# Optimization experiments

Measured on AMD Instinct MI355X. Metric: run time of the kernel, lower is better.

## Reference

```python
import jax, jax.numpy as jnp
import numpy as np

N = 50000      # nodes
E = 800000     # edges (avg degree 16)
IN_DIM = 256
OUT_DIM = 256
H = 8          # heads
HD = OUT_DIM // H  # head_dim = 32


def setup_inputs() -> dict:
    key = jax.random.key(0)
    k = jax.random.split(key, 6)
    x = jax.random.normal(k[0], (N, IN_DIM), jnp.float32)
    edge_index = jax.random.randint(k[1], (2, E), 0, N, dtype=jnp.int64)
    s = 1.0 / np.sqrt(IN_DIM)
    W_src = jax.random.normal(k[2], (IN_DIM, OUT_DIM), jnp.float32) * s
    W_dst = jax.random.normal(k[3], (IN_DIM, OUT_DIM), jnp.float32) * s
    b_src = jnp.zeros((OUT_DIM,), jnp.float32)
    b_dst = jnp.zeros((OUT_DIM,), jnp.float32)
    # xavier-ish scale for [H, 2*HD] attention vector
    attn_vec = jax.random.normal(k[4], (H, 2 * HD), jnp.float32) * np.sqrt(2.0 / (H + 2 * HD))
    return {"x": x, "edge_index": edge_index, "W_src": W_src, "b_src": b_src,
            "W_dst": W_dst, "b_dst": b_dst, "attn_vec": attn_vec}


def reference(x, edge_index, W_src, b_src, W_dst, b_dst, attn_vec):
    # Linear projections -> [N, H, HD]
    proj_src = (x @ W_src + b_src).reshape(N, H, HD)
    proj_dst = (x @ W_dst + b_dst).reshape(N, H, HD)
    # Split concat-dot into two per-node dot products (same math as
    # einsum('ehd,hd->eh', cat([src,dst]), attn_vec)), computed per node
    # then gathered per edge.
    a_src, a_dst = attn_vec[:, :HD], attn_vec[:, HD:]
    s_src = jnp.einsum('nhd,hd->nh', proj_src, a_src)  # [N, H]
    s_dst = jnp.einsum('nhd,hd->nh', proj_dst, a_dst)  # [N, H]
    e_src, e_dst = edge_index[0], edge_index[1]
    scores = s_src[e_src] + s_dst[e_dst]               # [E, H]
    scores = jnp.where(scores >= 0, scores, 0.2 * scores)  # LeakyReLU(0.2)
    # Segment softmax over destination nodes (original: exp / scatter-add(exp) + eps)
    ex = jnp.exp(scores)
    denom = jax.ops.segment_sum(ex, e_dst, num_segments=N)  # [N, H]
    alpha = ex / (denom[e_dst] + 1e-15)                     # [E, H]
    # Weighted scatter aggregation of src features
    weighted = alpha[:, :, None] * proj_src[e_src]          # [E, H, HD]
    agg = jax.ops.segment_sum(weighted, e_dst, num_segments=N)  # [N, H, HD]
    # Single relation -> mean over messages is identity; residual add
    return x + agg.reshape(N, OUT_DIM)
```

## Files before the change

### kernel.cpp

```cpp
#include <hip/hip_runtime.h>

#define DIM 256
#define NHEAD 8
#define HDIM 32
#define NCHUNK 256
#define SLOT 64

typedef __attribute__((ext_vector_type(4))) float f32x4;
typedef __attribute__((ext_vector_type(8))) short short8;
typedef __attribute__((ext_vector_type(8))) __bf16 bf16x8;

static __device__ __forceinline__ unsigned short f2bf(float f) {
  unsigned int u = __float_as_uint(f);
  u = (u + 0x7fffu + ((u >> 16) & 1u)) >> 16;
  return (unsigned short)u;
}

static __device__ __forceinline__ f32x4 mfma16x16x32(short8 a, short8 b, f32x4 c) {
  union { short8 s; bf16x8 b; } ua, ub;
  ua.s = a; ub.s = b;
  return __builtin_amdgcn_mfma_f32_16x16x32_bf16(ua.b, ub.b, c, 0, 0, 0);
}

static __device__ __forceinline__ int edge_at(const void* ei, int is64, long long pos) {
  if (is64) return (int)((const long long*)ei)[pos];
  return ((const int*)ei)[pos];
}

static __device__ __forceinline__ int detect64(const void* ei, int E, int tid) {
  const unsigned int* raw = (const unsigned int*)ei;
  int chk = E < 256 ? E : 256;
  int bad = 0;
  for (int i = tid & 63; i < chk; i += 64) bad |= (raw[2 * i + 1] != 0u);
  return (__ballot(bad) == 0ull);
}

__global__ void __launch_bounds__(256) k_prep(const float* Wsrc, const float* Wdst,
                       const float* bsrc, const float* bdst, const float* attn,
                       float* c16, unsigned short* wp,
                       const void* ei, int E, int CS, unsigned int* cnt8, int nw) {
  __shared__ unsigned int hist[12800];
  int b = blockIdx.x, tid = threadIdx.x;
  if (b < 256) {
    int idx = b * 256 + tid;
    int k = idx >> 8, n = idx & 255;
    int kb = k >> 5, khi = (k >> 3) & 3, i = k & 7;
    int ct = n >> 4, lane = khi * 16 + (n & 15);
    wp[(((size_t)ct * 8 + kb) * 64 + lane) * 8 + i] = f2bf(Wsrc[(size_t)k * DIM + n]);
  } else if (b == 256) {
    for (int q = tid * 16, qe = q + 16; q < qe; ++q) {
      int kb = q >> 9, lane = (q >> 3) & 63, i = q & 7;
      int k = kb * 32 + ((lane >> 4) * 8) + i;
      int j = lane & 15;
      int h = j & 7;
      const float* W = (j < 8) ? Wsrc : Wdst;
      const float* a = attn + h * 2 * HDIM + ((j < 8) ? 0 : HDIM);
      float acc = 0.f;
      #pragma unroll
      for (int d = 0; d < HDIM; ++d)
        acc += W[(size_t)k * DIM + h * HDIM + d] * a[d];
      wp[(((size_t)16 * 8 + kb) * 64 + lane) * 8 + i] = f2bf(acc);
    }
    if (tid < 16) {
      int j = tid, h = j & 7;
      const float* bb = (j < 8) ? bsrc : bdst;
      const float* a = attn + h * 2 * HDIM + ((j < 8) ? 0 : HDIM);
      float c = 0.f;
      for (int d = 0; d < HDIM; ++d) c += bb[h * HDIM + d] * a[d];
      c16[j] = c;
    }
  } else {
    int c = b - 257;
    for (int i = tid; i < nw; i += 256) hist[i] = 0u;
    int is64 = detect64(ei, E, tid);
    __syncthreads();
    int e0 = c * CS;
    int e1 = e0 + CS; if (e1 > E) e1 = E;
    for (int e = e0 + tid; e < e1; e += 256) {
      int d = edge_at(ei, is64, (long long)E + e);
      atomicAdd(&hist[d >> 2], 1u << ((d & 3) * 8));
    }
    __syncthreads();
    unsigned int* row = cnt8 + (size_t)c * nw;
    for (int i = tid; i < nw; i += 256) row[i] = hist[i];
  }
}

__global__ void __launch_bounds__(256) k_p2g(const unsigned int* cnt8, unsigned int* base8,
                                             int* deg32, int nw, int N, int PB,
                                             const float* x, const unsigned short* wp,
                                             const float* bsrc, const float* c16,
                                             unsigned short* pb, float* ssrc, float* sdst) {
  int tid = threadIdx.x;
  if ((int)blockIdx.x < PB) {
    int q = blockIdx.x * 256 + tid;
    if (q >= nw) return;
    unsigned int s0 = 0, s1 = 0, s2 = 0, s3 = 0;
    for (int c = 0; c < NCHUNK; ++c) {
      unsigned int v = cnt8[(size_t)c * nw + q];
      base8[(size_t)c * nw + q] = s0 | (s1 << 8) | (s2 << 16) | (s3 << 24);
      s0 += v & 255u; s1 += (v >> 8) & 255u; s2 += (v >> 16) & 255u; s3 += (v >> 24) & 255u;
    }
    int d = q * 4;
    if (d     < N) deg32[d    ] = (int)s0;
    if (d + 1 < N) deg32[d + 1] = (int)s1;
    if (d + 2 < N) deg32[d + 2] = (int)s2;
    if (d + 3 < N) deg32[d + 3] = (int)s3;
    return;
  }
  const int m0 = ((int)blockIdx.x - PB) * 64;
  const int lane = tid & 63;
  const int w = tid >> 6;
  const int l15 = lane & 15, lhi = lane >> 4;
  int arow = m0 + w * 16 + l15;
  if (arow > N - 1) arow = N - 1;
  const float* xr = x + (size_t)arow * DIM + lhi * 8;
  short8 af[8];
  #pragma unroll
  for (int kb = 0; kb < 8; ++kb) {
    f32x4 q0 = *(const f32x4*)(xr + kb * 32);
    f32x4 q1 = *(const f32x4*)(xr + kb * 32 + 4);
    short8 a;
    a[0] = f2bf(q0[0]); a[1] = f2bf(q0[1]); a[2] = f2bf(q0[2]); a[3] = f2bf(q0[3]);
    a[4] = f2bf(q1[0]); a[5] = f2bf(q1[1]); a[6] = f2bf(q1[2]); a[7] = f2bf(q1[3]);
    af[kb] = a;
  }
  const short8* wp8 = (const short8*)wp;
  #pragma unroll 1
  for (int ct = 0; ct < 17; ++ct) {
    f32x4 acc = {0.f, 0.f, 0.f, 0.f};
    #pragma unroll
    for (int kb = 0; kb < 8; ++kb)
      acc = mfma16x16x32(af[kb], wp8[(size_t)(ct * 8 + kb) * 64 + lane], acc);
    if (ct < 16) {
      int col = ct * 16 + l15;
      float bs = bsrc[col];
      #pragma unroll
      for (int qq = 0; qq < 4; ++qq) {
        int orow = m0 + w * 16 + lhi * 4 + qq;
        if (orow < N) pb[(size_t)orow * DIM + col] = f2bf(acc[qq] + bs);
      }
    } else {
      int j = l15;
      float cadd = c16[j];
      #pragma unroll
      for (int qq = 0; qq < 4; ++qq) {
        int orow = m0 + w * 16 + lhi * 4 + qq;
        if (orow < N) {
          float val = acc[qq] + cadd;
          if (j < 8) ssrc[(size_t)orow * 8 + j] = val;
          else       sdst[(size_t)orow * 8 + (j - 8)] = val;
        }
      }
    }
  }
}

__global__ void __launch_bounds__(256) k_p3(const void* ei, int E, int CS,
                                            const unsigned int* base8, unsigned short* bsiu,
                                            int nw) {
  __shared__ unsigned int hist[12800];
  int tid = threadIdx.x, c = blockIdx.x;
  for (int i = tid; i < nw; i += 256) hist[i] = 0u;
  int is64 = detect64(ei, E, tid);
  __syncthreads();
  const unsigned int* brow = base8 + (size_t)c * nw;
  int e0 = c * CS;
  int e1 = e0 + CS; if (e1 > E) e1 = E;
  for (int e = e0 + tid; e < e1; e += 256) {
    int s = edge_at(ei, is64, e);
    int d = edge_at(ei, is64, (long long)E + e);
    unsigned int sh = (d & 3) * 8u;
    unsigned int r = (atomicAdd(&hist[d >> 2], 1u << sh) >> sh) & 255u;
    unsigned int slot = ((brow[d >> 2] >> sh) & 255u) + r;
    if (slot < SLOT) bsiu[(size_t)d * SLOT + slot] = (unsigned short)s;
  }
}

#define LOADP(st, R, EF) do {                                                  \
    int _st2 = (st) * 2;                                                       \
    if (_st2 >= deg) { R.x = 0u; R.y = 0u; R.z = 0u; R.w = 0u; EF = 0.f; }     \
    else {                                                                     \
      int _idx = _st2 + half;                                                  \
      int _c = _idx < deg ? _idx : deg - 1;                                    \
      int _s = __shfl(myS, _c, 64);                                            \
      R = *(const uint4*)(pb + (size_t)_s * DIM + (size_t)l31 * 8);            \
      float _sc = ssrc[(size_t)_s * 8 + h] + sd;                               \
      _sc = _sc >= 0.f ? _sc : 0.2f * _sc;                                     \
      float _ev = __expf(_sc);                                                 \
      EF = (_idx < deg) ? _ev : 0.f;                                           \
    }                                                                          \
  } while (0)

#define COMPUTE(R, EF) do {                                                    \
    dsum += EF;                                                                \
    a0 = fmaf(EF, __uint_as_float(R.x << 16),         a0);                     \
    a1 = fmaf(EF, __uint_as_float(R.x & 0xffff0000u), a1);                     \
    a2 = fmaf(EF, __uint_as_float(R.y << 16),         a2);                     \
    a3 = fmaf(EF, __uint_as_float(R.y & 0xffff0000u), a3);                     \
    a4 = fmaf(EF, __uint_as_float(R.z << 16),         a4);                     \
    a5 = fmaf(EF, __uint_as_float(R.z & 0xffff0000u), a5);                     \
    a6 = fmaf(EF, __uint_as_float(R.w << 16),         a6);                     \
    a7 = fmaf(EF, __uint_as_float(R.w & 0xffff0000u), a7);                     \
  } while (0)

__global__ void __launch_bounds__(256) k_agg(const float* x, const unsigned short* pb,
                                             const float* ssrc, const float* sdst,
                                             const int* deg32, const unsigned short* bsi,
                                             float* out, int N) {
  int gw = (int)((blockIdx.x * 256 + threadIdx.x) >> 6);
  if (gw >= N) return;
  const int lane = threadIdx.x & 63;
  const int half = lane >> 5;
  const int l31 = lane & 31;
  const int h = l31 >> 2;
  const size_t obase = (size_t)gw * DIM + l31 * 8 + half * 4;
  int deg = deg32[gw]; if (deg > SLOT) deg = SLOT;
  if (deg == 0) {
    *(f32x4*)(out + obase) = *(const f32x4*)(x + obase);
    return;
  }
  const float sd = sdst[(size_t)gw * 8 + h];
  int myS = (int)bsi[(size_t)gw * SLOT + (lane < deg ? lane : deg - 1)];

  float a0 = 0.f, a1 = 0.f, a2 = 0.f, a3 = 0.f;
  float a4 = 0.f, a5 = 0.f, a6 = 0.f, a7 = 0.f;
  float dsum = 0.f;
  int stages = (deg + 1) >> 1;

  uint4 R0, R1, R2; float E0, E1, E2;
  LOADP(0, R0, E0);
  LOADP(1, R1, E1);
  LOADP(2, R2, E2);
  for (int t = 0; t < stages; t += 3) {
    COMPUTE(R0, E0); LOADP(t + 3, R0, E0);
    COMPUTE(R1, E1); LOADP(t + 4, R1, E1);
    COMPUTE(R2, E2); LOADP(t + 5, R2, E2);
  }

  a0 += __shfl_xor(a0, 32, 64);
  a1 += __shfl_xor(a1, 32, 64);
  a2 += __shfl_xor(a2, 32, 64);
  a3 += __shfl_xor(a3, 32, 64);
  a4 += __shfl_xor(a4, 32, 64);
  a5 += __shfl_xor(a5, 32, 64);
  a6 += __shfl_xor(a6, 32, 64);
  a7 += __shfl_xor(a7, 32, 64);
  dsum += __shfl_xor(dsum, 32, 64);

  float inv = 1.f / (dsum + 1e-15f);
  float s0 = half ? a4 : a0;
  float s1 = half ? a5 : a1;
  float s2 = half ? a6 : a2;
  float s3 = half ? a7 : a3;
  f32x4 xv = *(const f32x4*)(x + obase);
  f32x4 o;
  o[0] = xv[0] + s0 * inv;
  o[1] = xv[1] + s1 * inv;
  o[2] = xv[2] + s2 * inv;
  o[3] = xv[3] + s3 * inv;
  *(f32x4*)(out + obase) = o;
}

extern "C" void kernel_launch(void* const* d_in, const int* in_sizes, int n_in,
                              void* d_out, int out_size, void* d_ws, size_t ws_size,
                              hipStream_t stream) {
  const float* x    = (const float*)d_in[0];
  const void*  ei   = d_in[1];
  const float* Wsrc = (const float*)d_in[2];
  const float* bsrc = (const float*)d_in[3];
  const float* Wdst = (const float*)d_in[4];
  const float* bdst = (const float*)d_in[5];
  const float* attn = (const float*)d_in[6];
  const int N = in_sizes[0] / DIM;
  const int E = in_sizes[1] / 2;
  float* out = (float*)d_out;

  char* wsp = (char*)d_ws;
  size_t off = 0;
  auto alloc = [&](size_t b) { char* p = wsp + off; off += (b + 255) & ~(size_t)255; return (void*)p; };
  const int nw = (N + 3) >> 2;
  unsigned short* pb   = (unsigned short*)alloc((size_t)N * DIM * 2);
  unsigned short* wp   = (unsigned short*)alloc((size_t)17 * 8 * 64 * 8 * 2);
  float* c16   = (float*)alloc(16 * 4);
  float* ssrc  = (float*)alloc((size_t)N * 8 * 4);
  float* sdst  = (float*)alloc((size_t)N * 8 * 4);
  unsigned int* cnt8  = (unsigned int*)alloc((size_t)NCHUNK * nw * 4);
  unsigned int* base8 = (unsigned int*)alloc((size_t)NCHUNK * nw * 4);
  int* deg32 = (int*)alloc((size_t)N * 4);
  unsigned short* bsiu = (unsigned short*)alloc((size_t)N * SLOT * 2);

  const int CS = (E + NCHUNK - 1) / NCHUNK;

  k_prep<<<257 + NCHUNK, 256, 0, stream>>>(Wsrc, Wdst, bsrc, bdst, attn, c16, wp,
                                           ei, E, CS, cnt8, nw);
  const int PB = (nw + 255) / 256;
  const int GB = (N + 63) / 64;
  k_p2g<<<PB + GB, 256, 0, stream>>>(cnt8, base8, deg32, nw, N, PB,
                                     x, wp, bsrc, c16, pb, ssrc, sdst);
  k_p3<<<NCHUNK, 256, 0, stream>>>(ei, E, CS, base8, bsiu, nw);
  k_agg<<<(N + 3) / 4, 256, 0, stream>>>(x, pb, ssrc, sdst, deg32, bsiu, out, N);
}
```

Before: 178.2 us.

## Use compact CSR, precomputed softmax weights, and head-major per-head aggregation

Replaces the fixed 64-slot per-node source buckets with a compact CSR whose per-node offsets come from an atomic global counter. This removes the silent truncation of degrees above 64. A new kernel computes the softmax weights per edge and head into an alpha buffer. Projected features are stored head-major so a separate aggregation pass per head reads 32-wide slices, giving 8x more blocks. This adds an extra kernel launch and E*8 floats of alpha traffic. Each aggregation wave now uses only 16 lanes to load narrow 4-byte values, which may cut memory efficiency compared with the old 16-byte loads.

```diff
diff --git a/kernel.cpp b/kernel.cpp
--- a/kernel.cpp
+++ b/kernel.cpp
@@ -4,9 +4,9 @@
 #define NHEAD 8
 #define HDIM 32
 #define NCHUNK 256
-#define SLOT 64
 
 typedef __attribute__((ext_vector_type(4))) float f32x4;
+typedef __attribute__((ext_vector_type(2))) float f32x2;
 typedef __attribute__((ext_vector_type(8))) short short8;
 typedef __attribute__((ext_vector_type(8))) __bf16 bf16x8;
 
@@ -38,7 +38,8 @@
 __global__ void __launch_bounds__(256) k_prep(const float* Wsrc, const float* Wdst,
                        const float* bsrc, const float* bdst, const float* attn,
                        float* c16, unsigned short* wp,
-                       const void* ei, int E, int CS, unsigned int* cnt8, int nw) {
+                       const void* ei, int E, int CS, unsigned int* cb8, int nw,
+                       unsigned int* gcnt) {
   __shared__ unsigned int hist[12800];
   int b = blockIdx.x, tid = threadIdx.x;
   if (b < 256) {
@@ -48,6 +49,7 @@
     int ct = n >> 4, lane = khi * 16 + (n & 15);
     wp[(((size_t)ct * 8 + kb) * 64 + lane) * 8 + i] = f2bf(Wsrc[(size_t)k * DIM + n]);
   } else if (b == 256) {
+    if (tid == 0) *gcnt = 0u;
     for (int q = tid * 16, qe = q + 16; q < qe; ++q) {
       int kb = q >> 9, lane = (q >> 3) & 63, i = q & 7;
       int k = kb * 32 + ((lane >> 4) * 8) + i;
@@ -81,31 +83,33 @@
       atomicAdd(&hist[d >> 2], 1u << ((d & 3) * 8));
     }
     __syncthreads();
-    unsigned int* row = cnt8 + (size_t)c * nw;
+    unsigned int* row = cb8 + (size_t)c * nw;
     for (int i = tid; i < nw; i += 256) row[i] = hist[i];
   }
 }
 
-__global__ void __launch_bounds__(256) k_p2g(const unsigned int* cnt8, unsigned int* base8,
-                                             int* deg32, int nw, int N, int PB,
+__global__ void __launch_bounds__(256) k_p2g(unsigned int* cb8, unsigned int* offs,
+                                             int* deg32, unsigned int* gcnt,
+                                             int nw, int N, int PB,
                                              const float* x, const unsigned short* wp,
                                              const float* bsrc, const float* c16,
-                                             unsigned short* pb, float* ssrc, float* sdst) {
+                                             unsigned short* pbh, float* ssrc, float* sdst) {
   int tid = threadIdx.x;
   if ((int)blockIdx.x < PB) {
     int q = blockIdx.x * 256 + tid;
     if (q >= nw) return;
     unsigned int s0 = 0, s1 = 0, s2 = 0, s3 = 0;
     for (int c = 0; c < NCHUNK; ++c) {
-      unsigned int v = cnt8[(size_t)c * nw + q];
-      base8[(size_t)c * nw + q] = s0 | (s1 << 8) | (s2 << 16) | (s3 << 24);
+      unsigned int v = cb8[(size_t)c * nw + q];
+      cb8[(size_t)c * nw + q] = s0 | (s1 << 8) | (s2 << 16) | (s3 << 24);
       s0 += v & 255u; s1 += (v >> 8) & 255u; s2 += (v >> 16) & 255u; s3 += (v >> 24) & 255u;
     }
+    unsigned int base = atomicAdd(gcnt, s0 + s1 + s2 + s3);
     int d = q * 4;
-    if (d     < N) deg32[d    ] = (int)s0;
-    if (d + 1 < N) deg32[d + 1] = (int)s1;
-    if (d + 2 < N) deg32[d + 2] = (int)s2;
-    if (d + 3 < N) deg32[d + 3] = (int)s3;
+    if (d     < N) { offs[d    ] = base;               deg32[d    ] = (int)s0; }
+    if (d + 1 < N) { offs[d + 1] = base + s0;          deg32[d + 1] = (int)s1; }
+    if (d + 2 < N) { offs[d + 2] = base + s0 + s1;     deg32[d + 2] = (int)s2; }
+    if (d + 3 < N) { offs[d + 3] = base + s0 + s1 + s2; deg32[d + 3] = (int)s3; }
     return;
   }
   const int m0 = ((int)blockIdx.x - PB) * 64;
@@ -135,10 +139,11 @@
     if (ct < 16) {
       int col = ct * 16 + l15;
       float bs = bsrc[col];
+      int hh = col >> 5, c31 = col & 31;
       #pragma unroll
       for (int qq = 0; qq < 4; ++qq) {
         int orow = m0 + w * 16 + lhi * 4 + qq;
-        if (orow < N) pb[(size_t)orow * DIM + col] = f2bf(acc[qq] + bs);
+        if (orow < N) pbh[((size_t)hh * N + orow) * 32 + c31] = f2bf(acc[qq] + bs);
       }
     } else {
       int j = l15;
@@ -157,8 +162,8 @@
 }
 
 __global__ void __launch_bounds__(256) k_p3(const void* ei, int E, int CS,
-                                            const unsigned int* base8, unsigned short* bsiu,
-                                            int nw) {
+                                            const unsigned int* base8, const unsigned int* offs,
+                                            unsigned short* scsr, int nw) {
   __shared__ unsigned int hist[12800];
   int tid = threadIdx.x, c = blockIdx.x;
   for (int i = tid; i < nw; i += 256) hist[i] = 0u;
@@ -172,94 +177,118 @@
     int d = edge_at(ei, is64, (long long)E + e);
     unsigned int sh = (d & 3) * 8u;
     unsigned int r = (atomicAdd(&hist[d >> 2], 1u << sh) >> sh) & 255u;
-    unsigned int slot = ((brow[d >> 2] >> sh) & 255u) + r;
-    if (slot < SLOT) bsiu[(size_t)d * SLOT + slot] = (unsigned short)s;
-  }
-}
-
-#define LOADP(st, R, EF) do {                                                  \
-    int _st2 = (st) * 2;                                                       \
-    if (_st2 >= deg) { R.x = 0u; R.y = 0u; R.z = 0u; R.w = 0u; EF = 0.f; }     \
-    else {                                                                     \
-      int _idx = _st2 + half;                                                  \
-      int _c = _idx < deg ? _idx : deg - 1;                                    \
-      int _s = __shfl(myS, _c, 64);                                            \
-      R = *(const uint4*)(pb + (size_t)_s * DIM + (size_t)l31 * 8);            \
-      float _sc = ssrc[(size_t)_s * 8 + h] + sd;                               \
-      _sc = _sc >= 0.f ? _sc : 0.2f * _sc;                                     \
-      float _ev = __expf(_sc);                                                 \
-      EF = (_idx < deg) ? _ev : 0.f;                                           \
-    }                                                                          \
-  } while (0)
-
-#define COMPUTE(R, EF) do {                                                    \
-    dsum += EF;                                                                \
-    a0 = fmaf(EF, __uint_as_float(R.x << 16),         a0);                     \
-    a1 = fmaf(EF, __uint_as_float(R.x & 0xffff0000u), a1);                     \
-    a2 = fmaf(EF, __uint_as_float(R.y << 16),         a2);                     \
-    a3 = fmaf(EF, __uint_as_float(R.y & 0xffff0000u), a3);                     \
-    a4 = fmaf(EF, __uint_as_float(R.z << 16),         a4);                     \
-    a5 = fmaf(EF, __uint_as_float(R.z & 0xffff0000u), a5);                     \
-    a6 = fmaf(EF, __uint_as_float(R.w << 16),         a6);                     \
-    a7 = fmaf(EF, __uint_as_float(R.w & 0xffff0000u), a7);                     \
-  } while (0)
-
-__global__ void __launch_bounds__(256) k_agg(const float* x, const unsigned short* pb,
-                                             const float* ssrc, const float* sdst,
-                                             const int* deg32, const unsigned short* bsi,
-                                             float* out, int N) {
-  int gw = (int)((blockIdx.x * 256 + threadIdx.x) >> 6);
-  if (gw >= N) return;
+    unsigned int within = ((brow[d >> 2] >> sh) & 255u) + r;
+    scsr[offs[d] + within] = (unsigned short)s;
+  }
+}
+
+__global__ void __launch_bounds__(256) k_ex(const unsigned short* scsr, const unsigned int* offs,
+                                            const int* deg32, const float* ssrc, const float* sdst,
+                                            float* alpha, int N, int E) {
+  int node = blockIdx.x * 4 + (threadIdx.x >> 6);
+  int lane = threadIdx.x & 63;
+  if (node >= N) return;
+  int deg = deg32[node];
+  if (deg == 0) return;
+  unsigned int o0 = offs[node];
+  f32x4 sd0 = *(const f32x4*)(sdst + (size_t)node * 8);
+  f32x4 sd1 = *(const f32x4*)(sdst + (size_t)node * 8 + 4);
+  if (deg <= 64) {
+    int cl = lane < deg ? lane : deg - 1;
+    int s_l = (int)scsr[o0 + cl];
+    f32x4 g0 = *(const f32x4*)(ssrc + (size_t)s_l * 8);
+    f32x4 g1 = *(const f32x4*)(ssrc + (size_t)s_l * 8 + 4);
+    #pragma unroll
+    for (int h = 0; h < 8; ++h) {
+      float sc = (h < 4 ? g0[h] : g1[h - 4]) + (h < 4 ? sd0[h] : sd1[h - 4]);
+      sc = sc >= 0.f ? sc : 0.2f * sc;
+      float ex = __expf(sc);
+      float dsum = (lane < deg) ? ex : 0.f;
+      #pragma unroll
+      for (int dd = 1; dd < 64; dd <<= 1) dsum += __shfl_xor(dsum, dd, 64);
+      if (lane < deg) alpha[(size_t)h * E + o0 + lane] = ex / (dsum + 1e-15f);
+    }
+  } else {
+    for (int h = 0; h < 8; ++h) {
+      float sd = (h < 4) ? sd0[h] : sd1[h - 4];
+      float dsum = 0.f;
+      for (int b0 = 0; b0 < deg; b0 += 64) {
+        int sl = b0 + lane;
+        float ex = 0.f;
+        if (sl < deg) {
+          int s = (int)scsr[o0 + sl];
+          float sc = ssrc[(size_t)s * 8 + h] + sd;
+          sc = sc >= 0.f ? sc : 0.2f * sc;
+          ex = __expf(sc);
+        }
+        #pragma unroll
+        for (int dd = 1; dd < 64; dd <<= 1) ex += __shfl_xor(ex, dd, 64);
+        dsum += ex;
+      }
+      float inv = 1.f / (dsum + 1e-15f);
+      for (int b0 = 0; b0 < deg; b0 += 64) {
+        int sl = b0 + lane;
+        if (sl < deg) {
+          int s = (int)scsr[o0 + sl];
+          float sc = ssrc[(size_t)s * 8 + h] + sd;
+          sc = sc >= 0.f ? sc : 0.2f * sc;
+          alpha[(size_t)h * E + o0 + sl] = __expf(sc) * inv;
+        }
+      }
+    }
+  }
+}
+
+__global__ void __launch_bounds__(256) k_agg(const float* x, const unsigned short* pbh,
+                                             const unsigned short* scsr, const float* alpha,
+                                             const unsigned int* offs, const int* deg32,
+                                             float* out, int N, int E, int NB) {
+  int bid = (int)blockIdx.x;
+  int h = bid / NB;
+  int nb = bid - h * NB;
+  int node = nb * 4 + (threadIdx.x >> 6);
+  if (node >= N) return;
   const int lane = threadIdx.x & 63;
-  const int half = lane >> 5;
-  const int l31 = lane & 31;
-  const int h = l31 >> 2;
-  const size_t obase = (size_t)gw * DIM + l31 * 8 + half * 4;
-  int deg = deg32[gw]; if (deg > SLOT) deg = SLOT;
+  const size_t ob = (size_t)node * DIM + h * 32;
+  int deg = deg32[node];
   if (deg == 0) {
-    *(f32x4*)(out + obase) = *(const f32x4*)(x + obase);
+    if (lane < 16) {
+      f32x2 xv = *(const f32x2*)(x + ob + lane * 2);
+      *(f32x2*)(out + ob + lane * 2) = xv;
+    }
     return;
   }
-  const float sd = sdst[(size_t)gw * 8 + h];
-  int myS = (int)bsi[(size_t)gw * SLOT + (lane < deg ? lane : deg - 1)];
-
-  float a0 = 0.f, a1 = 0.f, a2 = 0.f, a3 = 0.f;
-  float a4 = 0.f, a5 = 0.f, a6 = 0.f, a7 = 0.f;
-  float dsum = 0.f;
-  int stages = (deg + 1) >> 1;
-
-  uint4 R0, R1, R2; float E0, E1, E2;
-  LOADP(0, R0, E0);
-  LOADP(1, R1, E1);
-  LOADP(2, R2, E2);
-  for (int t = 0; t < stages; t += 3) {
-    COMPUTE(R0, E0); LOADP(t + 3, R0, E0);
-    COMPUTE(R1, E1); LOADP(t + 4, R1, E1);
-    COMPUTE(R2, E2); LOADP(t + 5, R2, E2);
-  }
-
-  a0 += __shfl_xor(a0, 32, 64);
-  a1 += __shfl_xor(a1, 32, 64);
-  a2 += __shfl_xor(a2, 32, 64);
-  a3 += __shfl_xor(a3, 32, 64);
-  a4 += __shfl_xor(a4, 32, 64);
-  a5 += __shfl_xor(a5, 32, 64);
-  a6 += __shfl_xor(a6, 32, 64);
-  a7 += __shfl_xor(a7, 32, 64);
-  dsum += __shfl_xor(dsum, 32, 64);
-
-  float inv = 1.f / (dsum + 1e-15f);
-  float s0 = half ? a4 : a0;
-  float s1 = half ? a5 : a1;
-  float s2 = half ? a6 : a2;
-  float s3 = half ? a7 : a3;
-  f32x4 xv = *(const f32x4*)(x + obase);
-  f32x4 o;
-  o[0] = xv[0] + s0 * inv;
-  o[1] = xv[1] + s1 * inv;
-  o[2] = xv[2] + s2 * inv;
-  o[3] = xv[3] + s3 * inv;
-  *(f32x4*)(out + obase) = o;
+  unsigned int o0 = offs[node];
+  const unsigned short* slice = pbh + (size_t)h * N * 32;
+  const float* al = alpha + (size_t)h * E;
+  float acc0 = 0.f, acc1 = 0.f;
+  const int c2 = (lane & 15) * 2;
+  for (int b0 = 0; b0 < deg; b0 += 64) {
+    int nt = deg - b0; if (nt > 64) nt = 64;
+    int cl = lane < nt ? lane : nt - 1;
+    int myS = (int)scsr[o0 + b0 + cl];
+    float myA = al[o0 + b0 + cl];
+    for (int t = 0; t * 4 < nt; ++t) {
+      int idx = t * 4 + (lane >> 4);
+      int s = __shfl(myS, idx, 64);
+      float a = __shfl(myA, idx, 64);
+      a = (idx < nt) ? a : 0.f;
+      unsigned int v = *(const unsigned int*)(slice + (size_t)s * 32 + c2);
+      acc0 = fmaf(a, __uint_as_float(v << 16),         acc0);
+      acc1 = fmaf(a, __uint_as_float(v & 0xffff0000u), acc1);
+    }
+  }
+  acc0 += __shfl_xor(acc0, 16, 64);
+  acc0 += __shfl_xor(acc0, 32, 64);
+  acc1 += __shfl_xor(acc1, 16, 64);
+  acc1 += __shfl_xor(acc1, 32, 64);
+  if (lane < 16) {
+    f32x2 xv = *(const f32x2*)(x + ob + c2);
+    f32x2 o;
+    o[0] = xv[0] + acc0;
+    o[1] = xv[1] + acc1;
+    *(f32x2*)(out + ob + c2) = o;
+  }
 }
 
 extern "C" void kernel_launch(void* const* d_in, const int* in_sizes, int n_in,
@@ -280,24 +309,28 @@
   size_t off = 0;
   auto alloc = [&](size_t b) { char* p = wsp + off; off += (b + 255) & ~(size_t)255; return (void*)p; };
   const int nw = (N + 3) >> 2;
-  unsigned short* pb   = (unsigned short*)alloc((size_t)N * DIM * 2);
+  unsigned short* pbh  = (unsigned short*)alloc((size_t)N * DIM * 2);
   unsigned short* wp   = (unsigned short*)alloc((size_t)17 * 8 * 64 * 8 * 2);
   float* c16   = (float*)alloc(16 * 4);
   float* ssrc  = (float*)alloc((size_t)N * 8 * 4);
   float* sdst  = (float*)alloc((size_t)N * 8 * 4);
-  unsigned int* cnt8  = (unsigned int*)alloc((size_t)NCHUNK * nw * 4);
-  unsigned int* base8 = (unsigned int*)alloc((size_t)NCHUNK * nw * 4);
+  unsigned int* cb8  = (unsigned int*)alloc((size_t)NCHUNK * nw * 4);
+  unsigned int* offs = (unsigned int*)alloc((size_t)N * 4);
   int* deg32 = (int*)alloc((size_t)N * 4);
-  unsigned short* bsiu = (unsigned short*)alloc((size_t)N * SLOT * 2);
+  unsigned short* scsr = (unsigned short*)alloc((size_t)E * 2);
+  float* alpha = (float*)alloc((size_t)E * 8 * 4);
+  unsigned int* gcnt = (unsigned int*)alloc(256);
 
   const int CS = (E + NCHUNK - 1) / NCHUNK;
 
   k_prep<<<257 + NCHUNK, 256, 0, stream>>>(Wsrc, Wdst, bsrc, bdst, attn, c16, wp,
-                                           ei, E, CS, cnt8, nw);
+                                           ei, E, CS, cb8, nw, gcnt);
   const int PB = (nw + 255) / 256;
   const int GB = (N + 63) / 64;
-  k_p2g<<<PB + GB, 256, 0, stream>>>(cnt8, base8, deg32, nw, N, PB,
-                                     x, wp, bsrc, c16, pb, ssrc, sdst);
-  k_p3<<<NCHUNK, 256, 0, stream>>>(ei, E, CS, base8, bsiu, nw);
-  k_agg<<<(N + 3) / 4, 256, 0, stream>>>(x, pb, ssrc, sdst, deg32, bsiu, out, N);
-}
+  k_p2g<<<PB + GB, 256, 0, stream>>>(cb8, offs, deg32, gcnt, nw, N, PB,
+                                     x, wp, bsrc, c16, pbh, ssrc, sdst);
+  k_p3<<<NCHUNK, 256, 0, stream>>>(ei, E, CS, cb8, offs, scsr, nw);
+  const int XB = (N + 3) / 4;
+  k_ex<<<XB, 256, 0, stream>>>(scsr, offs, deg32, ssrc, sdst, alpha, N, E);
+  k_agg<<<8 * XB, 256, 0, stream>>>(x, pbh, scsr, alpha, offs, deg32, out, N, E, XB);
+}
```

Measured after the change: 309.9 us. +73.9%, slower.
